# Optimization experiments

Measured on AMD Instinct MI355X. Metric: run time of the kernel, lower is better.

Reference implementation:

```python
import jax, jax.numpy as jnp
import numpy as np

B, S, D_IN, D_OUT = 8, 4096, 512, 64

def setup_inputs() -> dict:
    key = jax.random.key(0)
    k1, k2, k3, k4 = jax.random.split(key, 4)
    scale = 1.0 / np.sqrt(D_IN)
    return {
        "x": jax.random.normal(k1, (B, S, D_IN), dtype=jnp.float32),
        "W_Q": jax.random.normal(k2, (D_IN, D_OUT), dtype=jnp.float32) * scale,
        "W_K": jax.random.normal(k3, (D_IN, D_OUT), dtype=jnp.float32) * scale,
        "W_V": jax.random.normal(k4, (D_IN, D_OUT), dtype=jnp.float32) * scale,
    }

def reference(x, W_Q, W_K, W_V):
    # q,k,v: [B,S,D_OUT]
    q = jnp.einsum("bsd,de->bse", x, W_Q)
    k = jnp.einsum("bsd,de->bse", x, W_K)
    v = jnp.einsum("bsd,de->bse", x, W_V)
    d_out = k.shape[-1]
    # scores: [B,S,S], causal mask (upper triangle -> -inf)
    scores = jnp.einsum("bqe,bke->bqk", q, k)
    s = q.shape[1]
    causal = jnp.tril(jnp.ones((s, s), dtype=bool))
    scores = jnp.where(causal[None, :, :], scores, -jnp.inf)
    attn = jax.nn.softmax(scores / jnp.sqrt(jnp.asarray(d_out, scores.dtype)), axis=-1)
    # dropout p=0.0 (eval) -> identity
    return jnp.einsum("bqk,bke->bqe", attn, v)
```

## Files before the change

### kernel.cpp

```cpp
#include <hip/hip_runtime.h>
#include <hip/hip_bf16.h>

#define B_    8
#define S_    4096
#define DIN   512
#define DOUT  64
#define NROWS (B_ * S_)

typedef __attribute__((ext_vector_type(8)))  short bf16x8;
typedef __attribute__((ext_vector_type(4)))  float f32x4;
typedef __attribute__((ext_vector_type(16))) float f32x16;
typedef __attribute__((ext_vector_type(2)))  unsigned int u32x2;
typedef __attribute__((ext_vector_type(2)))  int i32x2;

typedef const __attribute__((address_space(1))) unsigned int GUI;
typedef __attribute__((address_space(3))) unsigned int LUI;

__device__ __forceinline__ unsigned short f32_to_bf16(float f) {
    union { float f; unsigned int u; } c; c.f = f;
    unsigned int r = (c.u + 0x7FFFu + ((c.u >> 16) & 1u)) >> 16;
    return (unsigned short)r;
}
__device__ __forceinline__ float bf16_to_f32(unsigned short us) {
    union { unsigned int u; float f; } c; c.u = (unsigned int)us << 16;
    return c.f;
}

__device__ __forceinline__ float fast_exp2(float x) {
#if __has_builtin(__builtin_amdgcn_exp2f)
    return __builtin_amdgcn_exp2f(x);
#else
    return exp2f(x);
#endif
}

__device__ __forceinline__ float sum_xor32(float v) {
    i32x2 r = __builtin_amdgcn_permlane32_swap(__float_as_int(v), __float_as_int(v),
                                               false, false);
    return __int_as_float(r.x) + __int_as_float(r.y);
}

#define LDS_READS_DONE_FENCE() do {                                   \
    asm volatile("s_waitcnt lgkmcnt(0)" ::: "memory");                \
    __builtin_amdgcn_sched_barrier(0);                                \
} while (0)

__device__ __forceinline__ int pidx_of(int tp, int j) {
    if (tp < 16) return tp - 8;
    if (tp < 24) return 8 + (tp - 16) * 2 + (j - 1);
    return 24 + (tp - 24) * 3 + (j - 1);
}

#define PART_STRIDE 16896

__global__ void wt_convert(const float* __restrict__ WQ,
                           const float* __restrict__ WK,
                           const float* __restrict__ WV,
                           unsigned short* __restrict__ Wt2) {
    int idx = blockIdx.x * 256 + threadIdx.x;
    if (idx >= 3 * 512 * 16) return;
    int p   = idx / 8192;
    int rem = idx - p * 8192;
    int k   = rem >> 4;
    int n0  = (rem & 15) * 4;
    const float* W = (p == 0) ? WQ : ((p == 1) ? WK : WV);
    float4 v = *(const float4*)(W + k * 64 + n0);
    const int ks = k >> 5, kl = k & 31;
    float vv[4] = {v.x, v.y, v.z, v.w};
#pragma unroll
    for (int r = 0; r < 4; ++r) {
        int n = n0 + r;
        Wt2[(size_t)((ks * 12 + p * 4 + (n >> 4)) * 512) + (n & 15) * 32 + kl] =
            f32_to_bf16(vv[r]);
    }
}

__global__ __launch_bounds__(256) void qkv_proj(const float* __restrict__ x,
                                                const unsigned short* __restrict__ Wt2,
                                                unsigned short* __restrict__ QKV) {
    __shared__ alignas(16) float          xtile[2][1024];
    __shared__ alignas(16) unsigned short btile[2][6144];

    const int tid  = threadIdx.x;
    const int lane = tid & 63;
    const int wq   = tid >> 6;
    const int c15  = lane & 15;
    const int g    = lane >> 4;
    const float* xblk = x + (size_t)blockIdx.x * 32 * DIN;

    const int rw     = (wq & 1) * 16 + c15;
    const int nfbase = (wq >> 1) * 6;

    const int xrow = wq * 8 + (lane >> 3);
    const int xsl  = (lane & 7) ^ (xrow & 7);

    auto stage = [&](int slot, int ks) {
        __builtin_amdgcn_global_load_lds((GUI*)(xblk + ks * 32 + xrow * DIN + xsl * 4),
                                         (LUI*)((char*)&xtile[slot][0] + wq * 1024), 16, 0, 0);
        const unsigned short* Bs = Wt2 + (size_t)ks * 6144;
#pragma unroll
        for (int j = 0; j < 3; ++j)
            __builtin_amdgcn_global_load_lds((GUI*)(Bs + (j * 256 + tid) * 8),
                                             (LUI*)((char*)&btile[slot][0] + j * 4096 + wq * 1024),
                                             16, 0, 0);
    };
    stage(0, 0);
    stage(1, 1);

    f32x4 acc[6] = {};

    int cur = 0;
    for (int ks = 0; ks < 16; ++ks) {
        asm volatile("s_waitcnt vmcnt(4)" ::: "memory");
        asm volatile("s_barrier" ::: "memory");

        const char* xb = (const char*)&xtile[cur][0] + rw * 128;
        f32x4 a0 = *(const f32x4*)(xb + (((2 * g)     ^ (rw & 7)) << 4));
        f32x4 a1 = *(const f32x4*)(xb + (((2 * g + 1) ^ (rw & 7)) << 4));
        union { unsigned w[4]; bf16x8 v; } af;
        asm("v_cvt_pk_bf16_f32 %0, %1, %2" : "=v"(af.w[0]) : "v"(a0[0]), "v"(a0[1]));
        asm("v_cvt_pk_bf16_f32 %0, %1, %2" : "=v"(af.w[1]) : "v"(a0[2]), "v"(a0[3]));
        asm("v_cvt_pk_bf16_f32 %0, %1, %2" : "=v"(af.w[2]) : "v"(a1[0]), "v"(a1[1]));
        asm("v_cvt_pk_bf16_f32 %0, %1, %2" : "=v"(af.w[3]) : "v"(a1[2]), "v"(a1[3]));

        const char* bb = (const char*)&btile[cur][0] + c15 * 64 + g * 16;
#pragma unroll
        for (int n = 0; n < 6; ++n) {
            bf16x8 bf = *(const bf16x8*)(bb + (nfbase + n) * 1024);
            acc[n] = __builtin_amdgcn_mfma_f32_16x16x32_bf16(af.v, bf, acc[n], 0, 0, 0);
        }

        LDS_READS_DONE_FENCE();
        asm volatile("s_barrier" ::: "memory");
        {
            int tn = ks + 2; if (tn > 15) tn = 15;
            stage(cur, tn);
        }
        cur ^= 1;
    }
    asm volatile("s_waitcnt vmcnt(0)" ::: "memory");

    const int orow0 = blockIdx.x * 32 + (wq & 1) * 16 + g * 4;
#pragma unroll
    for (int n = 0; n < 6; ++n) {
        const int nfg  = nfbase + n;
        const int p    = nfg >> 2;
        const int ncol = (nfg & 3) * 16 + c15;
        if (p < 2) {
            unsigned short* outp = QKV + (size_t)p * NROWS * DOUT;
            const float sc = (p == 0) ? 0.125f * 1.44269504089f : 1.0f;
#pragma unroll
            for (int r = 0; r < 4; ++r)
                outp[(size_t)(orow0 + r) * DOUT + ncol] = f32_to_bf16(acc[n][r] * sc);
        } else {
            const int bb2  = orow0 >> 12;
            const int srow = orow0 & 4095;
            const int kb   = srow >> 5;
            const int kvl  = srow & 31;
            union { unsigned short s[4]; u32x2 d; } pk;
#pragma unroll
            for (int r = 0; r < 4; ++r) pk.s[r] = f32_to_bf16(acc[n][r]);
            *(u32x2*)(QKV + (size_t)2 * NROWS * DOUT + (size_t)bb2 * S_ * DOUT +
                      ((size_t)(kb * 4 + (kvl >> 3)) * 64 + ncol) * 8 + (kvl & 7)) = pk.d;
        }
    }
}

__global__ __launch_bounds__(512) void qk_norms(const unsigned short* __restrict__ QKV,
                                                float* __restrict__ qn,
                                                float* __restrict__ ktm) {
    __shared__ float lds[64];
    const int bid  = blockIdx.x;
    const bool isK = bid >= 512;
    const int blk  = isK ? bid - 512 : bid;
    const int tid  = threadIdx.x;
    const int rowl = tid >> 3;
    const int part = tid & 7;
    const size_t row = (size_t)blk * 64 + rowl;

    const unsigned short* src = QKV + (isK ? (size_t)NROWS * DOUT : 0) +
                                row * DOUT + part * 8;
    bf16x8 v = *(const bf16x8*)src;
    float s = 0.f;
#pragma unroll
    for (int i2 = 0; i2 < 8; ++i2) {
        float f = bf16_to_f32((unsigned short)v[i2]);
        s += f * f;
    }
    s += __shfl_xor(s, 1, 64);
    s += __shfl_xor(s, 2, 64);
    s += __shfl_xor(s, 4, 64);

    if (!isK) {
        if (part == 0) qn[row] = sqrtf(s);
    } else {
        if (part == 0) lds[rowl] = s;
        __syncthreads();
        if (tid < 64) {
            float m = lds[tid];
#pragma unroll
            for (int st = 32; st >= 1; st >>= 1)
                m = fmaxf(m, __shfl_xor(m, st, 64));
            if (tid == 0) ktm[blk] = sqrtf(m);
        }
    }
}

__global__ void kpref(const float* __restrict__ ktm, float* __restrict__ pm) {
    const int b = blockIdx.x;
    const int t = threadIdx.x;
    float m = 0.f;
    for (int u = 0; u <= t; ++u) m = fmaxf(m, ktm[b * 64 + u]);
    pm[b * 64 + t] = m;
}

__global__ __launch_bounds__(64) void attn_fwd(const unsigned short* __restrict__ QKV,
                                               const float* __restrict__ qn,
                                               const float* __restrict__ pm,
                                               float* __restrict__ out,
                                               char* __restrict__ part1,
                                               float* __restrict__ ml0) {
    __shared__ alignas(16) unsigned short k_lds[2][2048];
    __shared__ alignas(16) unsigned short v_lds[2][2048];

    const int bid = blockIdx.x;
    const int b   = bid & 7;
    const int w   = bid >> 3;
    const int qq  = w & 3;
    const int i   = 79 - (w >> 2);
    int tp, j;
    if      (i < 8)  { tp = i;                   j = 0; }
    else if (i < 24) { tp = 8 + ((i - 8) >> 1);  j = (i - 8) & 1; }
    else if (i < 48) { tp = 16 + (i - 24) / 3;   j = (i - 24) % 3; }
    else             { tp = 24 + ((i - 48) >> 2); j = (i - 48) & 3; }
    const int tile_hi = min(16 * j + 15, 2 * tp + 1);
    const int kb_lo   = 32 * j;
    const int kb_end  = min(2 * tile_hi + 1, 4 * tp + qq);

    const int lane = threadIdx.x;
    const int q31  = lane & 31;
    const int h    = lane >> 5;

    const unsigned short* Qg  = QKV + (size_t)b * S_ * DOUT;
    const unsigned short* Kg  = QKV + (size_t)NROWS * DOUT + (size_t)b * S_ * DOUT;
    const unsigned short* V2g = QKV + (size_t)2 * NROWS * DOUT + (size_t)b * S_ * DOUT;

    const int ql128 = qq * 32 + q31;
    const int qrow  = tp * 128 + ql128;
    const unsigned short* Qr = Qg + (size_t)qrow * DOUT + 8 * h;
    bf16x8 qf[4];
#pragma unroll
    for (int s = 0; s < 4; ++s) qf[s] = *(const bf16x8*)(Qr + 16 * s);

    const float M_r = qn[(size_t)b * S_ + qrow] * pm[b * 64 + (qrow >> 6)];
    asm volatile("s_waitcnt vmcnt(0)" ::: "memory");

    const int krow = lane >> 3;
    auto stage = [&](int slot, int kb) {
        const unsigned short* Kt = Kg + (size_t)kb * 2048;
        const unsigned short* Vt = V2g + (size_t)kb * 2048;
        char* kbase = (char*)&k_lds[slot][0];
        char* vbase = (char*)&v_lds[slot][0];
#pragma unroll
        for (int r = 0; r < 4; ++r) {
            const int row = r * 8 + krow;
            const int sl  = (lane & 7) ^ (row & 7);
            __builtin_amdgcn_global_load_lds((GUI*)(Kt + row * DOUT + sl * 8),
                                             (LUI*)(kbase + r * 1024), 16, 0, 0);
        }
#pragma unroll
        for (int r = 0; r < 4; ++r)
            __builtin_amdgcn_global_load_lds((GUI*)(Vt + (r * 64 + lane) * 8),
                                             (LUI*)(vbase + r * 1024), 16, 0, 0);
    };

    stage(0, kb_lo);
    stage(1, min(kb_lo + 1, kb_end));

    f32x16 oacc0 = {}, oacc1 = {};
    float l_r = 0.f;

    int cur = 0;
    for (int kb = kb_lo; kb <= kb_end; ++kb) {
        asm volatile("s_waitcnt vmcnt(8)" ::: "memory");

        const char* kb_ = (const char*)&k_lds[cur][0];
        const char* vb_ = (const char*)&v_lds[cur][0];

        f32x16 sA = {};
        __builtin_amdgcn_s_setprio(1);
#pragma unroll
        for (int s = 0; s < 4; ++s) {
            bf16x8 ka = *(const bf16x8*)(kb_ + q31 * 128 + (((2 * s + h) ^ (q31 & 7)) << 4));
            sA = __builtin_amdgcn_mfma_f32_32x32x16_bf16(ka, qf[s], sA, 0, 0, 0);
        }
        __builtin_amdgcn_s_setprio(0);

        if (kb >= 4 * tp + qq) {
#pragma unroll
            for (int r2 = 0; r2 < 16; ++r2) {
                const int kvg = 32 * kb + (r2 & 3) + 8 * (r2 >> 2) + 4 * h;
                if (kvg > qrow) sA[r2] = -1.0e30f;
            }
        }

        float t0 = 0.f, t1 = 0.f;
#pragma unroll
        for (int k2 = 0; k2 < 16; ++k2) sA[k2] = fast_exp2(sA[k2] - M_r);
#pragma unroll
        for (int k2 = 0; k2 < 8; ++k2) { t0 += sA[k2]; t1 += sA[k2 + 8]; }
        l_r += t0 + t1;

#define STEP_PV(u) do {                                                            \
        const int e0 = 2 * (u);                                                    \
        unsigned pa, pb2, pc, pd;                                                  \
        asm("v_cvt_pk_bf16_f32 %0, %1, %2" : "=v"(pa)  : "v"(sA[4*e0+0]), "v"(sA[4*e0+1])); \
        asm("v_cvt_pk_bf16_f32 %0, %1, %2" : "=v"(pb2) : "v"(sA[4*e0+2]), "v"(sA[4*e0+3])); \
        asm("v_cvt_pk_bf16_f32 %0, %1, %2" : "=v"(pc)  : "v"(sA[4*e0+4]), "v"(sA[4*e0+5])); \
        asm("v_cvt_pk_bf16_f32 %0, %1, %2" : "=v"(pd)  : "v"(sA[4*e0+6]), "v"(sA[4*e0+7])); \
        i32x2 ra = __builtin_amdgcn_permlane32_swap((int)pa,  (int)pc, false, false); \
        i32x2 rb = __builtin_amdgcn_permlane32_swap((int)pb2, (int)pd, false, false); \
        union { unsigned wv[4]; bf16x8 v; } pw;                                    \
        pw.wv[0] = (unsigned)ra.x; pw.wv[1] = (unsigned)rb.x;                      \
        pw.wv[2] = (unsigned)ra.y; pw.wv[3] = (unsigned)rb.y;                      \
        const int slot = 2 * (u) + h;                                              \
        bf16x8 vfa = *(const bf16x8*)(vb_ + slot * 1024 + q31 * 16);               \
        bf16x8 vfb = *(const bf16x8*)(vb_ + slot * 1024 + (32 + q31) * 16);        \
        oacc0 = __builtin_amdgcn_mfma_f32_32x32x16_bf16(vfa, pw.v, oacc0, 0, 0, 0);\
        oacc1 = __builtin_amdgcn_mfma_f32_32x32x16_bf16(vfb, pw.v, oacc1, 0, 0, 0);\
    } while (0)

        __builtin_amdgcn_s_setprio(1);
        STEP_PV(0); STEP_PV(1);
        __builtin_amdgcn_s_setprio(0);
#undef STEP_PV

        LDS_READS_DONE_FENCE();
        stage(cur, min(kb + 2, kb_end));
        cur ^= 1;
    }

    asm volatile("s_waitcnt vmcnt(0)" ::: "memory");

    l_r = sum_xor32(l_r);

    if (j == 0 && tp < 8) {
        const float linv = 1.0f / l_r;
        float* op = out + (size_t)b * S_ * DOUT + (size_t)qrow * DOUT;
#pragma unroll
        for (int e = 0; e < 4; ++e) {
            f32x4 v0 = { oacc0[4*e+0]*linv, oacc0[4*e+1]*linv, oacc0[4*e+2]*linv, oacc0[4*e+3]*linv };
            f32x4 v1 = { oacc1[4*e+0]*linv, oacc1[4*e+1]*linv, oacc1[4*e+2]*linv, oacc1[4*e+3]*linv };
            *(f32x4*)(op + 8*e + 4*h)      = v0;
            *(f32x4*)(op + 32 + 8*e + 4*h) = v1;
        }
    } else if (j == 0) {
        float* op = out + (size_t)b * S_ * DOUT + (size_t)qrow * DOUT;
#pragma unroll
        for (int e = 0; e < 4; ++e) {
            f32x4 v0 = { oacc0[4*e+0], oacc0[4*e+1], oacc0[4*e+2], oacc0[4*e+3] };
            f32x4 v1 = { oacc1[4*e+0], oacc1[4*e+1], oacc1[4*e+2], oacc1[4*e+3] };
            *(f32x4*)(op + 8*e + 4*h)      = v0;
            *(f32x4*)(op + 32 + 8*e + 4*h) = v1;
        }
        if (h == 0) ml0[(size_t)(b * 24 + (tp - 8)) * 128 + ql128] = l_r;
    } else {
        char* pb_ = part1 + (size_t)(b * 48 + pidx_of(tp, j)) * PART_STRIDE;
        if (h == 0) ((float*)pb_)[ql128] = l_r;
        unsigned short* ob = (unsigned short*)(pb_ + 512);
#pragma unroll
        for (int e = 0; e < 4; ++e) {
            union { unsigned short s[4]; u32x2 d; } k0, k1;
#pragma unroll
            for (int c = 0; c < 4; ++c) { k0.s[c] = f32_to_bf16(oacc0[4*e+c]);
                                          k1.s[c] = f32_to_bf16(oacc1[4*e+c]); }
            *(u32x2*)(ob + (size_t)ql128 * 64 + 8*e + 4*h)      = k0.d;
            *(u32x2*)(ob + (size_t)ql128 * 64 + 32 + 8*e + 4*h) = k1.d;
        }
    }
}

template<int NC>
__device__ __forceinline__ void reduce_body(int b, int tp, int q, int d,
                                            float* __restrict__ out,
                                            const char* __restrict__ part1,
                                            const float* __restrict__ ml0) {
    float* otile = out + ((size_t)b * S_ + (size_t)tp * 128) * 64;
    float L = ml0[(size_t)(b * 24 + (tp - 8)) * 128 + q];
    float O = otile[(size_t)q * 64 + d];
#pragma unroll
    for (int jj = 0; jj < NC - 1; ++jj) {
        const char* pb = part1 + (size_t)(b * 48 + pidx_of(tp, jj + 1)) * PART_STRIDE;
        L += ((const float*)pb)[q];
        O += bf16_to_f32(((const unsigned short*)(pb + 512))[(size_t)q * 64 + d]);
    }
    otile[(size_t)q * 64 + d] = O / L;
}

__global__ __launch_bounds__(256) void attn_reduce(float* __restrict__ out,
                                                   const char* __restrict__ part1,
                                                   const float* __restrict__ ml0) {
    const int bid = blockIdx.x;
    const int sub = bid & 31;
    const int tz  = (bid >> 5) % 24;
    const int b   = bid / (32 * 24);
    const int tp  = tz + 8;
    const int q   = sub * 4 + (threadIdx.x >> 6);
    const int d   = threadIdx.x & 63;

    if (tp < 16)      reduce_body<2>(b, tp, q, d, out, part1, ml0);
    else if (tp < 24) reduce_body<3>(b, tp, q, d, out, part1, ml0);
    else              reduce_body<4>(b, tp, q, d, out, part1, ml0);
}

extern "C" void kernel_launch(void* const* d_in, const int* in_sizes, int n_in,
                              void* d_out, int out_size, void* d_ws, size_t ws_size,
                              hipStream_t stream) {
    const float* x  = (const float*)d_in[0];
    const float* WQ = (const float*)d_in[1];
    const float* WK = (const float*)d_in[2];
    const float* WV = (const float*)d_in[3];

    unsigned short* Wt2   = (unsigned short*)d_ws;
    unsigned short* QKV   = Wt2 + 192 * 512;
    char*           part1 = (char*)d_ws + 12779520;
    float*          ml0   = (float*)((char*)d_ws + 19267584);
    float*          qn    = (float*)((char*)d_ws + 19365888);
    float*          ktm   = (float*)((char*)d_ws + 19496960);
    float*          pmb   = (float*)((char*)d_ws + 19499008);
    float* out = (float*)d_out;

    wt_convert<<<96, 256, 0, stream>>>(WQ, WK, WV, Wt2);
    qkv_proj<<<1024, 256, 0, stream>>>(x, Wt2, QKV);
    qk_norms<<<1024, 512, 0, stream>>>(QKV, qn, ktm);
    kpref<<<8, 64, 0, stream>>>(ktm, pmb);
    attn_fwd<<<2560, 64, 0, stream>>>(QKV, qn, pmb, out, part1, ml0);
    attn_reduce<<<6144, 256, 0, stream>>>(out, part1, ml0);
}
```

Before: 78.77 us.

## Process two 32-row query groups per wave to reuse staged K/V tiles

Each attention wave now handles 64 query rows (two 32-row groups) instead of 32, so every K/V tile staged into LDS feeds twice as many MFMAs. The grid is halved, which cuts redundant global-to-LDS K/V traffic. In exchange, register pressure roughly doubles (four output accumulators, two score tiles), there are fewer waves to hide latency, and the lower group does one extra masked diagonal block.

```diff
diff --git a/kernel.cpp b/kernel.cpp
--- a/kernel.cpp
+++ b/kernel.cpp
@@ -226,8 +226,8 @@
     const int bid = blockIdx.x;
     const int b   = bid & 7;
     const int w   = bid >> 3;
-    const int qq  = w & 3;
-    const int i   = 79 - (w >> 2);
+    const int qq2 = w & 1;
+    const int i   = 79 - (w >> 1);
     int tp, j;
     if      (i < 8)  { tp = i;                   j = 0; }
     else if (i < 24) { tp = 8 + ((i - 8) >> 1);  j = (i - 8) & 1; }
@@ -235,7 +235,8 @@
     else             { tp = 24 + ((i - 48) >> 2); j = (i - 48) & 3; }
     const int tile_hi = min(16 * j + 15, 2 * tp + 1);
     const int kb_lo   = 32 * j;
-    const int kb_end  = min(2 * tile_hi + 1, 4 * tp + qq);
+    const int kb_diagA = 4 * tp + 2 * qq2;
+    const int kb_end   = min(2 * tile_hi + 1, kb_diagA + 1);
 
     const int lane = threadIdx.x;
     const int q31  = lane & 31;
@@ -245,14 +246,23 @@
     const unsigned short* Kg  = QKV + (size_t)NROWS * DOUT + (size_t)b * S_ * DOUT;
     const unsigned short* V2g = QKV + (size_t)2 * NROWS * DOUT + (size_t)b * S_ * DOUT;
 
-    const int ql128 = qq * 32 + q31;
-    const int qrow  = tp * 128 + ql128;
-    const unsigned short* Qr = Qg + (size_t)qrow * DOUT + 8 * h;
-    bf16x8 qf[4];
-#pragma unroll
-    for (int s = 0; s < 4; ++s) qf[s] = *(const bf16x8*)(Qr + 16 * s);
-
-    const float M_r = qn[(size_t)b * S_ + qrow] * pm[b * 64 + (qrow >> 6)];
+    const int base   = tp * 128 + qq2 * 64;
+    const int qrowA  = base + q31;
+    const int qrowB  = base + 32 + q31;
+    bf16x8 qfA[4], qfB[4];
+    {
+        const unsigned short* QrA = Qg + (size_t)qrowA * DOUT + 8 * h;
+        const unsigned short* QrB = Qg + (size_t)qrowB * DOUT + 8 * h;
+#pragma unroll
+        for (int s = 0; s < 4; ++s) {
+            qfA[s] = *(const bf16x8*)(QrA + 16 * s);
+            qfB[s] = *(const bf16x8*)(QrB + 16 * s);
+        }
+    }
+
+    const float pmv = pm[b * 64 + (base >> 6)];
+    const float M_A = qn[(size_t)b * S_ + qrowA] * pmv;
+    const float M_B = qn[(size_t)b * S_ + qrowB] * pmv;
     asm volatile("s_waitcnt vmcnt(0)" ::: "memory");
 
     const int krow = lane >> 3;
@@ -277,8 +287,8 @@
     stage(0, kb_lo);
     stage(1, min(kb_lo + 1, kb_end));
 
-    f32x16 oacc0 = {}, oacc1 = {};
-    float l_r = 0.f;
+    f32x16 oA0 = {}, oA1 = {}, oB0 = {}, oB1 = {};
+    float lA = 0.f, lB = 0.f;
 
     int cur = 0;
     for (int kb = kb_lo; kb <= kb_end; ++kb) {
@@ -287,37 +297,42 @@
         const char* kb_ = (const char*)&k_lds[cur][0];
         const char* vb_ = (const char*)&v_lds[cur][0];
 
-        f32x16 sA = {};
+        f32x16 sA = {}, sB = {};
         __builtin_amdgcn_s_setprio(1);
 #pragma unroll
         for (int s = 0; s < 4; ++s) {
             bf16x8 ka = *(const bf16x8*)(kb_ + q31 * 128 + (((2 * s + h) ^ (q31 & 7)) << 4));
-            sA = __builtin_amdgcn_mfma_f32_32x32x16_bf16(ka, qf[s], sA, 0, 0, 0);
+            sA = __builtin_amdgcn_mfma_f32_32x32x16_bf16(ka, qfA[s], sA, 0, 0, 0);
+            sB = __builtin_amdgcn_mfma_f32_32x32x16_bf16(ka, qfB[s], sB, 0, 0, 0);
         }
         __builtin_amdgcn_s_setprio(0);
 
-        if (kb >= 4 * tp + qq) {
+        if (kb >= kb_diagA) {
 #pragma unroll
             for (int r2 = 0; r2 < 16; ++r2) {
                 const int kvg = 32 * kb + (r2 & 3) + 8 * (r2 >> 2) + 4 * h;
-                if (kvg > qrow) sA[r2] = -1.0e30f;
+                if (kvg > qrowA) sA[r2] = -1.0e30f;
+                if (kvg > qrowB) sB[r2] = -1.0e30f;
             }
         }
 
-        float t0 = 0.f, t1 = 0.f;
-#pragma unroll
-        for (int k2 = 0; k2 < 16; ++k2) sA[k2] = fast_exp2(sA[k2] - M_r);
-#pragma unroll
-        for (int k2 = 0; k2 < 8; ++k2) { t0 += sA[k2]; t1 += sA[k2 + 8]; }
-        l_r += t0 + t1;
-
-#define STEP_PV(u) do {                                                            \
+        float tA = 0.f, tB = 0.f;
+#pragma unroll
+        for (int k2 = 0; k2 < 16; ++k2) {
+            sA[k2] = fast_exp2(sA[k2] - M_A);
+            sB[k2] = fast_exp2(sB[k2] - M_B);
+        }
+#pragma unroll
+        for (int k2 = 0; k2 < 16; ++k2) { tA += sA[k2]; tB += sB[k2]; }
+        lA += tA; lB += tB;
+
+#define STEP_PV(u, Pv, oLo, oHi) do {                                              \
         const int e0 = 2 * (u);                                                    \
         unsigned pa, pb2, pc, pd;                                                  \
-        asm("v_cvt_pk_bf16_f32 %0, %1, %2" : "=v"(pa)  : "v"(sA[4*e0+0]), "v"(sA[4*e0+1])); \
-        asm("v_cvt_pk_bf16_f32 %0, %1, %2" : "=v"(pb2) : "v"(sA[4*e0+2]), "v"(sA[4*e0+3])); \
-        asm("v_cvt_pk_bf16_f32 %0, %1, %2" : "=v"(pc)  : "v"(sA[4*e0+4]), "v"(sA[4*e0+5])); \
-        asm("v_cvt_pk_bf16_f32 %0, %1, %2" : "=v"(pd)  : "v"(sA[4*e0+6]), "v"(sA[4*e0+7])); \
+        asm("v_cvt_pk_bf16_f32 %0, %1, %2" : "=v"(pa)  : "v"(Pv[4*e0+0]), "v"(Pv[4*e0+1])); \
+        asm("v_cvt_pk_bf16_f32 %0, %1, %2" : "=v"(pb2) : "v"(Pv[4*e0+2]), "v"(Pv[4*e0+3])); \
+        asm("v_cvt_pk_bf16_f32 %0, %1, %2" : "=v"(pc)  : "v"(Pv[4*e0+4]), "v"(Pv[4*e0+5])); \
+        asm("v_cvt_pk_bf16_f32 %0, %1, %2" : "=v"(pd)  : "v"(Pv[4*e0+6]), "v"(Pv[4*e0+7])); \
         i32x2 ra = __builtin_amdgcn_permlane32_swap((int)pa,  (int)pc, false, false); \
         i32x2 rb = __builtin_amdgcn_permlane32_swap((int)pb2, (int)pd, false, false); \
         union { unsigned wv[4]; bf16x8 v; } pw;                                    \
@@ -326,12 +341,13 @@
         const int slot = 2 * (u) + h;                                              \
         bf16x8 vfa = *(const bf16x8*)(vb_ + slot * 1024 + q31 * 16);               \
         bf16x8 vfb = *(const bf16x8*)(vb_ + slot * 1024 + (32 + q31) * 16);        \
-        oacc0 = __builtin_amdgcn_mfma_f32_32x32x16_bf16(vfa, pw.v, oacc0, 0, 0, 0);\
-        oacc1 = __builtin_amdgcn_mfma_f32_32x32x16_bf16(vfb, pw.v, oacc1, 0, 0, 0);\
+        oLo = __builtin_amdgcn_mfma_f32_32x32x16_bf16(vfa, pw.v, oLo, 0, 0, 0);    \
+        oHi = __builtin_amdgcn_mfma_f32_32x32x16_bf16(vfb, pw.v, oHi, 0, 0, 0);    \
     } while (0)
 
         __builtin_amdgcn_s_setprio(1);
-        STEP_PV(0); STEP_PV(1);
+        STEP_PV(0, sA, oA0, oA1); STEP_PV(1, sA, oA0, oA1);
+        STEP_PV(0, sB, oB0, oB1); STEP_PV(1, sB, oB0, oB1);
         __builtin_amdgcn_s_setprio(0);
 #undef STEP_PV
 
@@ -342,42 +358,48 @@
 
     asm volatile("s_waitcnt vmcnt(0)" ::: "memory");
 
-    l_r = sum_xor32(l_r);
-
-    if (j == 0 && tp < 8) {
-        const float linv = 1.0f / l_r;
-        float* op = out + (size_t)b * S_ * DOUT + (size_t)qrow * DOUT;
-#pragma unroll
-        for (int e = 0; e < 4; ++e) {
-            f32x4 v0 = { oacc0[4*e+0]*linv, oacc0[4*e+1]*linv, oacc0[4*e+2]*linv, oacc0[4*e+3]*linv };
-            f32x4 v1 = { oacc1[4*e+0]*linv, oacc1[4*e+1]*linv, oacc1[4*e+2]*linv, oacc1[4*e+3]*linv };
-            *(f32x4*)(op + 8*e + 4*h)      = v0;
-            *(f32x4*)(op + 32 + 8*e + 4*h) = v1;
-        }
-    } else if (j == 0) {
-        float* op = out + (size_t)b * S_ * DOUT + (size_t)qrow * DOUT;
-#pragma unroll
-        for (int e = 0; e < 4; ++e) {
-            f32x4 v0 = { oacc0[4*e+0], oacc0[4*e+1], oacc0[4*e+2], oacc0[4*e+3] };
-            f32x4 v1 = { oacc1[4*e+0], oacc1[4*e+1], oacc1[4*e+2], oacc1[4*e+3] };
-            *(f32x4*)(op + 8*e + 4*h)      = v0;
-            *(f32x4*)(op + 32 + 8*e + 4*h) = v1;
-        }
-        if (h == 0) ml0[(size_t)(b * 24 + (tp - 8)) * 128 + ql128] = l_r;
-    } else {
-        char* pb_ = part1 + (size_t)(b * 48 + pidx_of(tp, j)) * PART_STRIDE;
-        if (h == 0) ((float*)pb_)[ql128] = l_r;
-        unsigned short* ob = (unsigned short*)(pb_ + 512);
-#pragma unroll
-        for (int e = 0; e < 4; ++e) {
-            union { unsigned short s[4]; u32x2 d; } k0, k1;
-#pragma unroll
-            for (int c = 0; c < 4; ++c) { k0.s[c] = f32_to_bf16(oacc0[4*e+c]);
-                                          k1.s[c] = f32_to_bf16(oacc1[4*e+c]); }
-            *(u32x2*)(ob + (size_t)ql128 * 64 + 8*e + 4*h)      = k0.d;
-            *(u32x2*)(ob + (size_t)ql128 * 64 + 32 + 8*e + 4*h) = k1.d;
-        }
-    }
+    lA = sum_xor32(lA);
+    lB = sum_xor32(lB);
+
+    const int qlA = qq2 * 64 + q31;
+    const int qlB = qlA + 32;
+
+#define WRITE_GROUP(oLo, oHi, lR, qrow, ql128) do {                                \
+    if (j == 0 && tp < 8) {                                                        \
+        const float linv = 1.0f / (lR);                                            \
+        float* op = out + (size_t)b * S_ * DOUT + (size_t)(qrow) * DOUT;           \
+        for (int e = 0; e < 4; ++e) {                                              \
+            f32x4 v0 = { oLo[4*e+0]*linv, oLo[4*e+1]*linv, oLo[4*e+2]*linv, oLo[4*e+3]*linv }; \
+            f32x4 v1 = { oHi[4*e+0]*linv, oHi[4*e+1]*linv, oHi[4*e+2]*linv, oHi[4*e+3]*linv }; \
+            *(f32x4*)(op + 8*e + 4*h)      = v0;                                   \
+            *(f32x4*)(op + 32 + 8*e + 4*h) = v1;                                   \
+        }                                                                          \
+    } else if (j == 0) {                                                           \
+        float* op = out + (size_t)b * S_ * DOUT + (size_t)(qrow) * DOUT;           \
+        for (int e = 0; e < 4; ++e) {                                              \
+            f32x4 v0 = { oLo[4*e+0], oLo[4*e+1], oLo[4*e+2], oLo[4*e+3] };         \
+            f32x4 v1 = { oHi[4*e+0], oHi[4*e+1], oHi[4*e+2], oHi[4*e+3] };         \
+            *(f32x4*)(op + 8*e + 4*h)      = v0;                                   \
+            *(f32x4*)(op + 32 + 8*e + 4*h) = v1;                                   \
+        }                                                                          \
+        if (h == 0) ml0[(size_t)(b * 24 + (tp - 8)) * 128 + (ql128)] = (lR);       \
+    } else {                                                                       \
+        char* pb_ = part1 + (size_t)(b * 48 + pidx_of(tp, j)) * PART_STRIDE;       \
+        if (h == 0) ((float*)pb_)[(ql128)] = (lR);                                 \
+        unsigned short* ob = (unsigned short*)(pb_ + 512);                         \
+        for (int e = 0; e < 4; ++e) {                                              \
+            union { unsigned short s[4]; u32x2 d; } k0, k1;                        \
+            for (int c = 0; c < 4; ++c) { k0.s[c] = f32_to_bf16(oLo[4*e+c]);       \
+                                          k1.s[c] = f32_to_bf16(oHi[4*e+c]); }     \
+            *(u32x2*)(ob + (size_t)(ql128) * 64 + 8*e + 4*h)      = k0.d;          \
+            *(u32x2*)(ob + (size_t)(ql128) * 64 + 32 + 8*e + 4*h) = k1.d;          \
+        }                                                                          \
+    }                                                                              \
+} while (0)
+
+    WRITE_GROUP(oA0, oA1, lA, qrowA, qlA);
+    WRITE_GROUP(oB0, oB1, lB, qrowB, qlB);
+#undef WRITE_GROUP
 }
 
 template<int NC>
@@ -434,6 +456,6 @@
     qkv_proj<<<1024, 256, 0, stream>>>(x, Wt2, QKV);
     qk_norms<<<1024, 512, 0, stream>>>(QKV, qn, ktm);
     kpref<<<8, 64, 0, stream>>>(ktm, pmb);
-    attn_fwd<<<2560, 64, 0, stream>>>(QKV, qn, pmb, out, part1, ml0);
+    attn_fwd<<<1280, 64, 0, stream>>>(QKV, qn, pmb, out, part1, ml0);
     attn_reduce<<<6144, 256, 0, stream>>>(out, part1, ml0);
 }
```

Measured after the change: 84.58 us. +7.4%, slower.

## Store K in MFMA-fragment layout and load K/V directly into registers

Applied to the files above, without the earlier changes.

The projection kernel now writes K in a blocked layout that matches the attention MFMA operand fragments, and the norm kernel reads K through that layout. The attention kernel drops the LDS double buffer and async global-to-LDS staging. It instead loads the K and V fragments straight from global memory into registers, prefetching one block ahead. This removes LDS traffic and the barrier-like fences, but relies on the caches to serve repeated K/V reads across waves and adds register pressure.

```diff
diff --git a/kernel.cpp b/kernel.cpp
--- a/kernel.cpp
+++ b/kernel.cpp
@@ -146,12 +146,22 @@
         const int nfg  = nfbase + n;
         const int p    = nfg >> 2;
         const int ncol = (nfg & 3) * 16 + c15;
-        if (p < 2) {
-            unsigned short* outp = QKV + (size_t)p * NROWS * DOUT;
-            const float sc = (p == 0) ? 0.125f * 1.44269504089f : 1.0f;
+        if (p == 0) {
+            unsigned short* outp = QKV;
+            const float sc = 0.125f * 1.44269504089f;
 #pragma unroll
             for (int r = 0; r < 4; ++r)
                 outp[(size_t)(orow0 + r) * DOUT + ncol] = f32_to_bf16(acc[n][r] * sc);
+        } else if (p == 1) {
+            const int bb2  = orow0 >> 12;
+            const int srow = orow0 & 4095;
+            unsigned short* kbase = QKV + (size_t)NROWS * DOUT + (size_t)bb2 * S_ * DOUT;
+#pragma unroll
+            for (int r = 0; r < 4; ++r) {
+                const int sr = srow + r;
+                kbase[(((size_t)(sr >> 5) * 8 + (ncol >> 3)) * 32 + (sr & 31)) * 8 +
+                      (ncol & 7)] = f32_to_bf16(acc[n][r]);
+            }
         } else {
             const int bb2  = orow0 >> 12;
             const int srow = orow0 & 4095;
@@ -176,10 +186,16 @@
     const int tid  = threadIdx.x;
     const int rowl = tid >> 3;
     const int part = tid & 7;
-    const size_t row = (size_t)blk * 64 + rowl;
-
-    const unsigned short* src = QKV + (isK ? (size_t)NROWS * DOUT : 0) +
-                                row * DOUT + part * 8;
+
+    const unsigned short* src;
+    if (!isK) {
+        src = QKV + ((size_t)blk * 64 + rowl) * DOUT + part * 8;
+    } else {
+        const int b2  = blk >> 6;
+        const int srow = (blk & 63) * 64 + rowl;
+        src = QKV + (size_t)NROWS * DOUT + (size_t)b2 * S_ * DOUT +
+              (((size_t)(srow >> 5) * 8 + part) * 32 + (srow & 31)) * 8;
+    }
     bf16x8 v = *(const bf16x8*)src;
     float s = 0.f;
 #pragma unroll
@@ -192,7 +208,7 @@
     s += __shfl_xor(s, 4, 64);
 
     if (!isK) {
-        if (part == 0) qn[row] = sqrtf(s);
+        if (part == 0) qn[(size_t)blk * 64 + rowl] = sqrtf(s);
     } else {
         if (part == 0) lds[rowl] = s;
         __syncthreads();
@@ -220,9 +236,6 @@
                                                float* __restrict__ out,
                                                char* __restrict__ part1,
                                                float* __restrict__ ml0) {
-    __shared__ alignas(16) unsigned short k_lds[2][2048];
-    __shared__ alignas(16) unsigned short v_lds[2][2048];
-
     const int bid = blockIdx.x;
     const int b   = bid & 7;
     const int w   = bid >> 3;
@@ -242,7 +255,7 @@
     const int h    = lane >> 5;
 
     const unsigned short* Qg  = QKV + (size_t)b * S_ * DOUT;
-    const unsigned short* Kg  = QKV + (size_t)NROWS * DOUT + (size_t)b * S_ * DOUT;
+    const unsigned short* K2g = QKV + (size_t)NROWS * DOUT + (size_t)b * S_ * DOUT;
     const unsigned short* V2g = QKV + (size_t)2 * NROWS * DOUT + (size_t)b * S_ * DOUT;
 
     const int ql128 = qq * 32 + q31;
@@ -253,47 +266,42 @@
     for (int s = 0; s < 4; ++s) qf[s] = *(const bf16x8*)(Qr + 16 * s);
 
     const float M_r = qn[(size_t)b * S_ + qrow] * pm[b * 64 + (qrow >> 6)];
-    asm volatile("s_waitcnt vmcnt(0)" ::: "memory");
-
-    const int krow = lane >> 3;
-    auto stage = [&](int slot, int kb) {
-        const unsigned short* Kt = Kg + (size_t)kb * 2048;
-        const unsigned short* Vt = V2g + (size_t)kb * 2048;
-        char* kbase = (char*)&k_lds[slot][0];
-        char* vbase = (char*)&v_lds[slot][0];
-#pragma unroll
-        for (int r = 0; r < 4; ++r) {
-            const int row = r * 8 + krow;
-            const int sl  = (lane & 7) ^ (row & 7);
-            __builtin_amdgcn_global_load_lds((GUI*)(Kt + row * DOUT + sl * 8),
-                                             (LUI*)(kbase + r * 1024), 16, 0, 0);
-        }
-#pragma unroll
-        for (int r = 0; r < 4; ++r)
-            __builtin_amdgcn_global_load_lds((GUI*)(Vt + (r * 64 + lane) * 8),
-                                             (LUI*)(vbase + r * 1024), 16, 0, 0);
-    };
-
-    stage(0, kb_lo);
-    stage(1, min(kb_lo + 1, kb_end));
+
+    const unsigned short* Kl = K2g + ((size_t)(2 * 0 + h) * 32 + q31) * 8;
+    const unsigned short* Vl = V2g + (size_t)h * 512 + q31 * 8;
+
+#define LOAD_K(kr, kb) do {                                                   \
+    const unsigned short* kbp = Kl + (size_t)(kb) * 2048;                     \
+    kr[0] = *(const bf16x8*)(kbp);                                            \
+    kr[1] = *(const bf16x8*)(kbp + 512);                                      \
+    kr[2] = *(const bf16x8*)(kbp + 1024);                                     \
+    kr[3] = *(const bf16x8*)(kbp + 1536);                                     \
+} while (0)
+#define LOAD_V(vr, kb) do {                                                   \
+    const unsigned short* vbp = Vl + (size_t)(kb) * 2048;                     \
+    vr[0] = *(const bf16x8*)(vbp);                                            \
+    vr[1] = *(const bf16x8*)(vbp + 256);                         \
+    vr[2] = *(const bf16x8*)(vbp + 1024);                         \
+    vr[3] = *(const bf16x8*)(vbp + 1280);                                     \
+} while (0)
+
+    bf16x8 kc[4], vc[4], kn[4], vn[4];
+    LOAD_K(kc, kb_lo);
+    LOAD_V(vc, kb_lo);
 
     f32x16 oacc0 = {}, oacc1 = {};
     float l_r = 0.f;
 
-    int cur = 0;
     for (int kb = kb_lo; kb <= kb_end; ++kb) {
-        asm volatile("s_waitcnt vmcnt(8)" ::: "memory");
-
-        const char* kb_ = (const char*)&k_lds[cur][0];
-        const char* vb_ = (const char*)&v_lds[cur][0];
+        const int kbn = min(kb + 1, kb_end);
+        LOAD_K(kn, kbn);
+        LOAD_V(vn, kbn);
 
         f32x16 sA = {};
         __builtin_amdgcn_s_setprio(1);
 #pragma unroll
-        for (int s = 0; s < 4; ++s) {
-            bf16x8 ka = *(const bf16x8*)(kb_ + q31 * 128 + (((2 * s + h) ^ (q31 & 7)) << 4));
-            sA = __builtin_amdgcn_mfma_f32_32x32x16_bf16(ka, qf[s], sA, 0, 0, 0);
-        }
+        for (int s = 0; s < 4; ++s)
+            sA = __builtin_amdgcn_mfma_f32_32x32x16_bf16(kc[s], qf[s], sA, 0, 0, 0);
         __builtin_amdgcn_s_setprio(0);
 
         if (kb >= 4 * tp + qq) {
@@ -323,11 +331,8 @@
         union { unsigned wv[4]; bf16x8 v; } pw;                                    \
         pw.wv[0] = (unsigned)ra.x; pw.wv[1] = (unsigned)rb.x;                      \
         pw.wv[2] = (unsigned)ra.y; pw.wv[3] = (unsigned)rb.y;                      \
-        const int slot = 2 * (u) + h;                                              \
-        bf16x8 vfa = *(const bf16x8*)(vb_ + slot * 1024 + q31 * 16);               \
-        bf16x8 vfb = *(const bf16x8*)(vb_ + slot * 1024 + (32 + q31) * 16);        \
-        oacc0 = __builtin_amdgcn_mfma_f32_32x32x16_bf16(vfa, pw.v, oacc0, 0, 0, 0);\
-        oacc1 = __builtin_amdgcn_mfma_f32_32x32x16_bf16(vfb, pw.v, oacc1, 0, 0, 0);\
+        oacc0 = __builtin_amdgcn_mfma_f32_32x32x16_bf16(vc[2*(u)],   pw.v, oacc0, 0, 0, 0);\
+        oacc1 = __builtin_amdgcn_mfma_f32_32x32x16_bf16(vc[2*(u)+1], pw.v, oacc1, 0, 0, 0);\
     } while (0)
 
         __builtin_amdgcn_s_setprio(1);
@@ -335,12 +340,11 @@
         __builtin_amdgcn_s_setprio(0);
 #undef STEP_PV
 
-        LDS_READS_DONE_FENCE();
-        stage(cur, min(kb + 2, kb_end));
-        cur ^= 1;
-    }
-
-    asm volatile("s_waitcnt vmcnt(0)" ::: "memory");
+#pragma unroll
+        for (int z = 0; z < 4; ++z) { kc[z] = kn[z]; vc[z] = vn[z]; }
+    }
+#undef LOAD_K
+#undef LOAD_V
 
     l_r = sum_xor32(l_r);
 
```

New measurement: 79.18 us. About the same (+0.5%).
